# Optimization experiments

Measured on AMD Instinct MI355X. Metric: run time of the kernel, lower is better.

## Reference

```python
import jax, jax.numpy as jnp
import numpy as np

B, H, W = 512, 36, 36
N = H * W          # 1296 oscillators
K = 8              # couplings per oscillator
EP0 = 0.1          # kura_update_rate
ANNEAL = 0.5


def setup_inputs() -> dict:
    key = jax.random.key(0)
    k = jax.random.split(key, 8)
    return {
        "input": jax.random.normal(k[0], (B, H, W), jnp.float32),
        "initial_phase": jax.random.uniform(k[1], (B, N), jnp.float32) * (2.0 * np.pi),
        "connectivity": jax.random.randint(k[2], (B, N, K), 0, N),
        "episodes": 25,
        "conv1_w": jax.random.normal(k[3], (8, 1, 3, 3), jnp.float32) * 0.1,
        "conv1_b": jnp.zeros((8,), jnp.float32),
        "conv2_w": jax.random.normal(k[4], (16, 8, 3, 3), jnp.float32) * 0.1,
        "conv2_b": jnp.zeros((16,), jnp.float32),
        "conv3_w": jax.random.normal(k[5], (32, 16, 3, 3), jnp.float32) * 0.1,
        "conv3_b": jnp.zeros((32,), jnp.float32),
        "fc_w": jax.random.normal(k[6], (108 * 8, 108 * 32), jnp.float32) * 0.02,
        "fc_b": jnp.zeros((108 * 8,), jnp.float32),
    }


def _conv3x3(x, w, b):
    y = jax.lax.conv_general_dilated(
        x, w, (1, 1), "SAME", dimension_numbers=("NCHW", "OIHW", "NCHW"))
    return y + b[None, :, None, None]


def _kuramoto(initial_phase, coupling, connectivity, steps, ep0):
    # phase: [B,N]; coupling: [B,N,K]; connectivity: [B,N,K] neighbor indices
    gather = jax.vmap(lambda p, c: p[c])  # -> [B,N,K] neighbor phases

    def step(carry, i):
        phase, ep = carry
        neigh = gather(phase, connectivity)
        # d(phase_i) = ep * sum_j coupling_ij * sin(phase_j - phase_i)
        delta = ep * (coupling * jnp.sin(neigh - phase[:, :, None])).sum(-1)
        phase = phase + delta
        ep = ep - ANNEAL * i * ep / steps  # annealed update rate
        return (phase, ep), phase

    (_, _), phases = jax.lax.scan(
        step, (initial_phase, jnp.float32(ep0)),
        jnp.arange(steps, dtype=jnp.float32))
    # record=True: trajectory includes the initial phase
    return jnp.concatenate([initial_phase[None], phases], axis=0)  # [steps+1,B,N]


def reference(input, initial_phase, connectivity, episodes,
              conv1_w, conv1_b, conv2_w, conv2_b, conv3_w, conv3_b, fc_w, fc_b):
    x = input.reshape(-1, 1, 36, 36)
    c1 = jax.nn.relu(_conv3x3(x, conv1_w, conv1_b))
    c2 = jax.nn.relu(_conv3x3(c1, conv2_w, conv2_b))
    c3 = jax.nn.sigmoid(_conv3x3(c2, conv3_w, conv3_b))
    fc = (c3.reshape(-1, 108 * 32) @ fc_w.T + fc_b).reshape(-1, N, K)  # [B,1296,8]
    phase_list = _kuramoto(initial_phase, fc, connectivity, episodes, EP0)
    return phase_list, fc
```

## Files before the change

### kernel.cpp

```cpp
#include <hip/hip_runtime.h>
#include <hip/hip_bf16.h>

#define NPOS 1296
#define BATCH 512
#define STEPS 25
#define PH_STRIDE (BATCH * NPOS)
#define PH_TOTAL ((STEPS + 1) * PH_STRIDE)
#define FC_K 3456
#define FC_N 864
#define FC_NPAD 896
#define FC_M 6144

typedef float f32x4 __attribute__((ext_vector_type(4)));
typedef __bf16 bf16x8 __attribute__((ext_vector_type(8)));

__device__ __forceinline__ ushort f2bf(float f) {
  union { float f; unsigned u; } v; v.f = f;
  unsigned r = v.u + 0x7FFFu + ((v.u >> 16) & 1u);
  return (ushort)(r >> 16);
}
__device__ __forceinline__ float bf2f(ushort h) {
  union { unsigned u; float f; } v; v.u = ((unsigned)h) << 16; return v.f;
}

__device__ __forceinline__ void async_copy16(void* lds, const void* g) {
  __builtin_amdgcn_global_load_lds(
      (const __attribute__((address_space(1))) unsigned*)g,
      (__attribute__((address_space(3))) unsigned*)lds, 16, 0, 0);
}

__global__ __launch_bounds__(256) void wprep_kernel(
    const float* __restrict__ w1, const float* __restrict__ w2, const float* __restrict__ w3,
    float* __restrict__ w1t, ushort* __restrict__ w2t, ushort* __restrict__ w3t) {
  const int tid = threadIdx.x;
  for (int i = tid; i < 72; i += 256) {
    const int s = i / 8, co = i - s * 8;
    w1t[i] = w1[co * 9 + s];
  }
  for (int i = tid; i < 16 * 96; i += 256) {
    const int co = i / 96, k = i - co * 96;
    const int s = k / 8, ci = k - s * 8;
    w2t[i] = (k < 72) ? f2bf(w2[(co * 8 + ci) * 9 + s]) : (ushort)0;
  }
  for (int i = tid; i < 32 * 160; i += 256) {
    const int co = i / 160, k = i - co * 160;
    const int s = k / 16, ci = k - s * 16;
    w3t[i] = (k < 144) ? f2bf(w3[(co * 16 + ci) * 9 + s]) : (ushort)0;
  }
}

__global__ __launch_bounds__(256, 4) void conv_fused_kernel(
    const float* __restrict__ in, const float* __restrict__ w1t, const float* __restrict__ b1,
    const ushort* __restrict__ w2t, const float* __restrict__ b2,
    const ushort* __restrict__ w3t, const float* __restrict__ b3,
    ushort* __restrict__ aout) {
  __shared__ __align__(16) float sIn[18][40];
  __shared__ __align__(16) ushort sC1[18][40][8];
  __shared__ __align__(16) ushort sC2[16][40][16];
  const int b = blockIdx.x, band = blockIdx.y, tid = threadIdx.x;
  const int r0 = band * 12;
  const int wave = tid >> 6, lane = tid & 63;
  const int quad = lane >> 4, l16 = lane & 15;
  {
    const uint4 zz = make_uint4(0, 0, 0, 0);
    for (int i = tid; i < 180; i += 256) ((uint4*)sIn)[i] = zz;
    for (int i = tid; i < 720; i += 256) ((uint4*)sC1)[i] = zz;
    for (int i = tid; i < 1280; i += 256) ((uint4*)sC2)[i] = zz;
  }
  __syncthreads();
  for (int i = tid; i < 18 * 18; i += 256) {
    const int r = i / 18, c = i - r * 18;
    const int gy = r0 - 3 + r;
    if ((unsigned)gy < 36u)
      *(float2*)&sIn[r][2 + 2 * c] = *(const float2*)(in + (size_t)b * NPOS + gy * 36 + 2 * c);
  }
  __syncthreads();
  for (int i = tid; i < 16 * 36; i += 256) {
    const int lr = i / 36, x = i - lr * 36;
    float acc[8];
#pragma unroll
    for (int co = 0; co < 8; ++co) acc[co] = b1[co];
#pragma unroll
    for (int s = 0; s < 9; ++s) {
      const int dy = s / 3, dx = s - 3 * dy;
      const float v = sIn[lr + dy][x + 1 + dx];
#pragma unroll
      for (int co = 0; co < 8; ++co) acc[co] = fmaf(w1t[s * 8 + co], v, acc[co]);
    }
    const int g1 = r0 - 2 + lr;
    if ((unsigned)g1 < 36u) {
      uint4 pk;
      pk.x = (uint)f2bf(fmaxf(acc[0], 0.f)) | ((uint)f2bf(fmaxf(acc[1], 0.f)) << 16);
      pk.y = (uint)f2bf(fmaxf(acc[2], 0.f)) | ((uint)f2bf(fmaxf(acc[3], 0.f)) << 16);
      pk.z = (uint)f2bf(fmaxf(acc[4], 0.f)) | ((uint)f2bf(fmaxf(acc[5], 0.f)) << 16);
      pk.w = (uint)f2bf(fmaxf(acc[6], 0.f)) | ((uint)f2bf(fmaxf(acc[7], 0.f)) << 16);
      *(uint4*)&sC1[lr][x + 2][0] = pk;
    }
  }
  __syncthreads();
  bf16x8 w2f[3];
#pragma unroll
  for (int f = 0; f < 3; ++f)
    w2f[f] = *(const bf16x8*)(w2t + l16 * 96 + f * 32 + quad * 8);
  const float bias2 = b2[l16];
  for (int chunk = wave; chunk < 32; chunk += 4) {
    const int m = chunk * 16 + l16;
    const int oy = m / 36, x = m - oy * 36;
    f32x4 acc = {0.f, 0.f, 0.f, 0.f};
#pragma unroll
    for (int f = 0; f < 3; ++f) {
      const int s0 = 4 * f + quad;
      const int dy = s0 / 3, dx = s0 - 3 * dy;
      const bf16x8 af = *(const bf16x8*)&sC1[oy + dy][x + 1 + dx][0];
      acc = __builtin_amdgcn_mfma_f32_16x16x32_bf16(af, w2f[f], acc, 0, 0, 0);
    }
#pragma unroll
    for (int r = 0; r < 4; ++r) {
      const int px = chunk * 16 + quad * 4 + r;
      const int oy2 = px / 36, x2 = px - oy2 * 36;
      const int g2 = r0 - 1 + oy2;
      if (px < 504 && (unsigned)g2 < 36u)
        sC2[oy2][x2 + 2][l16] = f2bf(fmaxf(acc[r] + bias2, 0.f));
    }
  }
  __syncthreads();
  bf16x8 w3f[2][5];
#pragma unroll
  for (int t = 0; t < 2; ++t)
#pragma unroll
    for (int f = 0; f < 5; ++f)
      w3f[t][f] = *(const bf16x8*)(w3t + (t * 16 + l16) * 160 + f * 32 + quad * 8);
  const float bias3a = b3[l16], bias3b = b3[16 + l16];
  ushort* ob = aout + (size_t)b * (32 * NPOS) + r0 * 36;
  for (int chunk = wave; chunk < 27; chunk += 4) {
    const int m = chunk * 16 + l16;
    const int oy = m / 36, x = m - oy * 36;
    f32x4 acc0 = {0.f, 0.f, 0.f, 0.f}, acc1 = {0.f, 0.f, 0.f, 0.f};
#pragma unroll
    for (int f = 0; f < 5; ++f) {
      const int s0 = 2 * f + (quad >> 1);
      const int dy = s0 / 3, dx = s0 - 3 * dy;
      const bf16x8 af = *(const bf16x8*)&sC2[oy + dy][x + 1 + dx][(quad & 1) * 8];
      acc0 = __builtin_amdgcn_mfma_f32_16x16x32_bf16(af, w3f[0][f], acc0, 0, 0, 0);
      acc1 = __builtin_amdgcn_mfma_f32_16x16x32_bf16(af, w3f[1][f], acc1, 0, 0, 0);
    }
    const int pxb = chunk * 16 + quad * 4;
    ushort4 pk;
#pragma unroll
    for (int r = 0; r < 4; ++r)
      ((ushort*)&pk)[r] = f2bf(1.f / (1.f + __expf(-(acc0[r] + bias3a))));
    *(ushort4*)(ob + (size_t)l16 * NPOS + pxb) = pk;
#pragma unroll
    for (int r = 0; r < 4; ++r)
      ((ushort*)&pk)[r] = f2bf(1.f / (1.f + __expf(-(acc1[r] + bias3b))));
    *(ushort4*)(ob + (size_t)(16 + l16) * NPOS + pxb) = pk;
  }
}

__global__ __launch_bounds__(256) void wcvt_kernel(const float* __restrict__ w, ushort* __restrict__ wb) {
  const int idx = blockIdx.x * 256 + threadIdx.x;
  if (idx >= FC_NPAD * FC_K) return;
  const int n = idx / FC_K;
  wb[idx] = (n < FC_N) ? f2bf(w[idx]) : (ushort)0;
}

__global__ __launch_bounds__(256) void gemm_kernel(
    const ushort* __restrict__ A, const ushort* __restrict__ Bt,
    const float* __restrict__ bias, float* __restrict__ C) {
  __shared__ __align__(16) ushort sA[2][96 * 32];
  __shared__ __align__(16) ushort sB[2][128 * 32];
  const int tid = threadIdx.x;
  const int lin = blockIdx.x;
  const int xcd = lin & 7, g = lin >> 3;
  const int bn = g % 7;
  const int bm = xcd + 8 * (g / 7);
  const int row0 = bm * 96, col0 = bn * 128;
  const int wave = tid >> 6, lane = tid & 63;
  const int wr = (wave >> 1) * 48, wc = (wave & 1) * 64;
  const int quad = lane >> 4, l16 = lane & 15;
  f32x4 acc[3][4] = {};
  const ushort* Asrc  = A  + ((size_t)row0 + (tid >> 2)) * FC_K + (tid & 3) * 8;
  const ushort* Asrc2 = Asrc + (size_t)64 * FC_K;
  const ushort* Bsrc  = Bt + ((size_t)col0 + (tid >> 2)) * FC_K + (tid & 3) * 8;
  const ushort* Bsrc2 = Bsrc + (size_t)64 * FC_K;
  const int halfwave = (tid < 128);
  for (int kt = 0; kt < FC_K / 64; ++kt) {
    const int k0 = kt * 64;
    __syncthreads();
#pragma unroll
    for (int s = 0; s < 2; ++s) {
      const int off = k0 + s * 32;
      async_copy16(sA[s] + wave * 512, Asrc + off);
      async_copy16(sB[s] + wave * 512, Bsrc + off);
      async_copy16(sB[s] + 2048 + wave * 512, Bsrc2 + off);
      if (halfwave) async_copy16(sA[s] + 2048 + wave * 512, Asrc2 + off);
    }
    __syncthreads();
#pragma unroll
    for (int s = 0; s < 2; ++s) {
      bf16x8 af[3], bfr[4];
#pragma unroll
      for (int t = 0; t < 3; ++t)
        af[t] = *(const bf16x8*)(sA[s] + (wr + t * 16 + l16) * 32 + quad * 8);
#pragma unroll
      for (int t = 0; t < 4; ++t)
        bfr[t] = *(const bf16x8*)(sB[s] + (wc + t * 16 + l16) * 32 + quad * 8);
#pragma unroll
      for (int tm = 0; tm < 3; ++tm)
#pragma unroll
        for (int tn = 0; tn < 4; ++tn)
          acc[tm][tn] = __builtin_amdgcn_mfma_f32_16x16x32_bf16(af[tm], bfr[tn], acc[tm][tn], 0, 0, 0);
    }
  }
#pragma unroll
  for (int tn = 0; tn < 4; ++tn) {
    const int col = col0 + wc + tn * 16 + l16;
    if (col < FC_N) {
      const float bv = bias[col];
#pragma unroll
      for (int tm = 0; tm < 3; ++tm) {
#pragma unroll
        for (int r = 0; r < 4; ++r) {
          const int row = row0 + wr + tm * 16 + quad * 4 + r;
          C[(size_t)row * FC_N + col] = acc[tm][tn][r] + bv;
        }
      }
    }
  }
}

__global__ __launch_bounds__(512) void kuramoto_kernel(
    const float* __restrict__ ph0, const int* __restrict__ conn,
    const float* __restrict__ cpl, float* __restrict__ out) {
  __shared__ float ph[NPOS];
  __shared__ float2 sc[NPOS];
  const int b = blockIdx.x, tid = threadIdx.x;
  int rj[3][8];
  float rc[3][8];
#pragma unroll
  for (int s = 0; s < 3; ++s) {
    const int i = tid + s * 512;
    if (i < NPOS) {
      const float p = ph0[(size_t)b * NPOS + i];
      ph[i] = p;
      __builtin_nontemporal_store(p, out + (size_t)b * NPOS + i);
      const size_t base = (size_t)b * (NPOS * 8) + (size_t)i * 8;
      const int4 j0 = *(const int4*)(conn + base);
      const int4 j1 = *(const int4*)(conn + base + 4);
      const float4 c0 = *(const float4*)(cpl + base);
      const float4 c1 = *(const float4*)(cpl + base + 4);
      rj[s][0] = j0.x; rj[s][1] = j0.y; rj[s][2] = j0.z; rj[s][3] = j0.w;
      rj[s][4] = j1.x; rj[s][5] = j1.y; rj[s][6] = j1.z; rj[s][7] = j1.w;
      rc[s][0] = c0.x; rc[s][1] = c0.y; rc[s][2] = c0.z; rc[s][3] = c0.w;
      rc[s][4] = c1.x; rc[s][5] = c1.y; rc[s][6] = c1.z; rc[s][7] = c1.w;
    } else {
#pragma unroll
      for (int k = 0; k < 8; ++k) { rj[s][k] = 0; rc[s][k] = 0.f; }
    }
  }
  float ep = 0.1f;
  for (int t = 0; t < STEPS; ++t) {
    __syncthreads();
    for (int i = tid; i < NPOS; i += 512) {
      float s, c;
      __sincosf(ph[i], &s, &c);
      sc[i] = make_float2(s, c);
    }
    __syncthreads();
    float* op = out + (size_t)(t + 1) * PH_STRIDE + (size_t)b * NPOS;
#pragma unroll
    for (int s = 0; s < 3; ++s) {
      const int i = tid + s * 512;
      if (i < NPOS) {
        float ss = 0.f, cs = 0.f;
#pragma unroll
        for (int k = 0; k < 8; ++k) {
          const float2 v = sc[rj[s][k]];
          ss = fmaf(rc[s][k], v.x, ss);
          cs = fmaf(rc[s][k], v.y, cs);
        }
        const float2 me = sc[i];
        const float np = ph[i] + ep * (me.y * ss - me.x * cs);
        ph[i] = np;
        __builtin_nontemporal_store(np, op + i);
      }
    }
    ep = ep * (1.0f - 0.02f * (float)t);
  }
}

extern "C" void kernel_launch(void* const* d_in, const int* in_sizes, int n_in,
                              void* d_out, int out_size, void* d_ws, size_t ws_size,
                              hipStream_t stream) {
  const float* input = (const float*)d_in[0];
  const float* ph0   = (const float*)d_in[1];
  const int*   conn  = (const int*)d_in[2];
  const float* w1 = (const float*)d_in[4];
  const float* b1 = (const float*)d_in[5];
  const float* w2 = (const float*)d_in[6];
  const float* b2 = (const float*)d_in[7];
  const float* w3 = (const float*)d_in[8];
  const float* b3 = (const float*)d_in[9];
  const float* fcw = (const float*)d_in[10];
  const float* fcb = (const float*)d_in[11];
  float* out = (float*)d_out;

  ushort* Abuf = (ushort*)d_ws;
  ushort* Wbuf = (ushort*)((char*)d_ws + 42467328);
  float*  w1t  = (float*)((char*)d_ws + 48660480);
  ushort* w2t  = (ushort*)((char*)d_ws + 48660768);
  ushort* w3t  = (ushort*)((char*)d_ws + 48663840);
  float* fcout = out + PH_TOTAL;

  wprep_kernel<<<1, 256, 0, stream>>>(w1, w2, w3, w1t, w2t, w3t);
  wcvt_kernel<<<(FC_NPAD * FC_K) / 256, 256, 0, stream>>>(fcw, Wbuf);
  conv_fused_kernel<<<dim3(BATCH, 3), 256, 0, stream>>>(input, w1t, b1, w2t, b2, w3t, b3, Abuf);
  gemm_kernel<<<448, 256, 0, stream>>>(Abuf, Wbuf, fcb, fcout);
  kuramoto_kernel<<<BATCH, 512, 0, stream>>>(ph0, conn, fcout, out);
}
```

Baseline: 268.8 us.

## Pipeline GEMM loads with vmcnt waits and swizzled LDS; double-buffer Kuramoto sincos

The GEMM now keeps two K-tiles in flight. It issues global-to-LDS copies for tile k+2 right after computing tile k, and it waits with s_waitcnt vmcnt(7) plus a raw barrier instead of two full __syncthreads. It also XOR-swizzles the LDS layout to cut bank conflicts. The Kuramoto kernel keeps each oscillator's phase and sin/cos in registers and writes sin/cos into a ping-pong LDS buffer. This removes one barrier and the separate sincos pass per step. The wrap-around prefetch loads redundant tiles at the end, and the hand-written waitcnt logic depends on the compiler not reordering the memory operations.

```diff
diff --git a/kernel.cpp b/kernel.cpp
--- a/kernel.cpp
+++ b/kernel.cpp
@@ -10,6 +10,7 @@
 #define FC_N 864
 #define FC_NPAD 896
 #define FC_M 6144
+#define KT_ITERS 54
 
 typedef float f32x4 __attribute__((ext_vector_type(4)));
 typedef __bf16 bf16x8 __attribute__((ext_vector_type(8)));
@@ -28,6 +29,9 @@
       (const __attribute__((address_space(1))) unsigned*)g,
       (__attribute__((address_space(3))) unsigned*)lds, 16, 0, 0);
 }
+__device__ __forceinline__ void raw_barrier() { asm volatile("s_barrier" ::: "memory"); }
+__device__ __forceinline__ void waitcnt_vm7() { asm volatile("s_waitcnt vmcnt(7)" ::: "memory"); }
+__device__ __forceinline__ void waitcnt_vm0() { asm volatile("s_waitcnt vmcnt(0)" ::: "memory"); }
 
 __global__ __launch_bounds__(256) void wprep_kernel(
     const float* __restrict__ w1, const float* __restrict__ w2, const float* __restrict__ w3,
@@ -167,8 +171,7 @@
 __global__ __launch_bounds__(256) void gemm_kernel(
     const ushort* __restrict__ A, const ushort* __restrict__ Bt,
     const float* __restrict__ bias, float* __restrict__ C) {
-  __shared__ __align__(16) ushort sA[2][96 * 32];
-  __shared__ __align__(16) ushort sB[2][128 * 32];
+  __shared__ __align__(16) ushort smem[2][14336];
   const int tid = threadIdx.x;
   const int lin = blockIdx.x;
   const int xcd = lin & 7, g = lin >> 3;
@@ -178,40 +181,65 @@
   const int wave = tid >> 6, lane = tid & 63;
   const int wr = (wave >> 1) * 48, wc = (wave & 1) * 64;
   const int quad = lane >> 4, l16 = lane & 15;
+  const int oswz = (quad ^ ((l16 >> 1) & 3)) * 8;
   f32x4 acc[3][4] = {};
-  const ushort* Asrc  = A  + ((size_t)row0 + (tid >> 2)) * FC_K + (tid & 3) * 8;
-  const ushort* Asrc2 = Asrc + (size_t)64 * FC_K;
-  const ushort* Bsrc  = Bt + ((size_t)col0 + (tid >> 2)) * FC_K + (tid & 3) * 8;
-  const ushort* Bsrc2 = Bsrc + (size_t)64 * FC_K;
-  const int halfwave = (tid < 128);
-  for (int kt = 0; kt < FC_K / 64; ++kt) {
-    const int k0 = kt * 64;
-    __syncthreads();
-#pragma unroll
-    for (int s = 0; s < 2; ++s) {
-      const int off = k0 + s * 32;
-      async_copy16(sA[s] + wave * 512, Asrc + off);
-      async_copy16(sB[s] + wave * 512, Bsrc + off);
-      async_copy16(sB[s] + 2048 + wave * 512, Bsrc2 + off);
-      if (halfwave) async_copy16(sA[s] + 2048 + wave * 512, Asrc2 + off);
-    }
-    __syncthreads();
+
+  const int rr = lane >> 2;
+  const int soct = ((lane & 3) ^ ((lane >> 3) & 3)) * 8;
+  const ushort* gsrc[7];
+  const ushort* ldst[7];
+  {
+    const int s = wave >> 1;
+    if ((wave & 1) == 0) {
+#pragma unroll
+      for (int j = 0; j < 6; ++j) {
+        gsrc[j] = A + ((size_t)row0 + j * 16 + rr) * FC_K + s * 32 + soct;
+        ldst[j] = &smem[0][s * 3072 + j * 512];
+      }
+      gsrc[6] = Bt + ((size_t)col0 + rr) * FC_K + s * 32 + soct;
+      ldst[6] = &smem[0][6144 + s * 4096];
+    } else {
+#pragma unroll
+      for (int j = 0; j < 7; ++j) {
+        gsrc[j] = Bt + ((size_t)col0 + (j + 1) * 16 + rr) * FC_K + s * 32 + soct;
+        ldst[j] = &smem[0][6144 + s * 4096 + (j + 1) * 512];
+      }
+    }
+  }
+#pragma unroll
+  for (int j = 0; j < 7; ++j) async_copy16((void*)ldst[j], gsrc[j]);
+#pragma unroll
+  for (int j = 0; j < 7; ++j) async_copy16((void*)(ldst[j] + 14336), gsrc[j] + 64);
+
+  for (int kt = 0; kt < KT_ITERS; ++kt) {
+    const int p = kt & 1;
+    waitcnt_vm7();
+    raw_barrier();
+    const ushort* base = &smem[p][0];
 #pragma unroll
     for (int s = 0; s < 2; ++s) {
       bf16x8 af[3], bfr[4];
 #pragma unroll
       for (int t = 0; t < 3; ++t)
-        af[t] = *(const bf16x8*)(sA[s] + (wr + t * 16 + l16) * 32 + quad * 8);
+        af[t] = *(const bf16x8*)(base + s * 3072 + (wr + t * 16 + l16) * 32 + oswz);
 #pragma unroll
       for (int t = 0; t < 4; ++t)
-        bfr[t] = *(const bf16x8*)(sB[s] + (wc + t * 16 + l16) * 32 + quad * 8);
+        bfr[t] = *(const bf16x8*)(base + 6144 + s * 4096 + (wc + t * 16 + l16) * 32 + oswz);
 #pragma unroll
       for (int tm = 0; tm < 3; ++tm)
 #pragma unroll
         for (int tn = 0; tn < 4; ++tn)
           acc[tm][tn] = __builtin_amdgcn_mfma_f32_16x16x32_bf16(af[tm], bfr[tn], acc[tm][tn], 0, 0, 0);
     }
-  }
+    raw_barrier();
+    int kn = kt + 2;
+    if (kn >= KT_ITERS) kn -= KT_ITERS;
+    const int koff = kn * 64;
+#pragma unroll
+    for (int j = 0; j < 7; ++j) async_copy16((void*)(ldst[j] + p * 14336), gsrc[j] + koff);
+  }
+  waitcnt_vm0();
+
 #pragma unroll
   for (int tn = 0; tn < 4; ++tn) {
     const int col = col0 + wc + tn * 16 + l16;
@@ -232,18 +260,23 @@
 __global__ __launch_bounds__(512) void kuramoto_kernel(
     const float* __restrict__ ph0, const int* __restrict__ conn,
     const float* __restrict__ cpl, float* __restrict__ out) {
-  __shared__ float ph[NPOS];
-  __shared__ float2 sc[NPOS];
+  __shared__ float2 sc[2][NPOS];
   const int b = blockIdx.x, tid = threadIdx.x;
   int rj[3][8];
   float rc[3][8];
+  float myph[3];
+  float2 mysc[3];
 #pragma unroll
   for (int s = 0; s < 3; ++s) {
     const int i = tid + s * 512;
     if (i < NPOS) {
       const float p = ph0[(size_t)b * NPOS + i];
-      ph[i] = p;
+      myph[s] = p;
       __builtin_nontemporal_store(p, out + (size_t)b * NPOS + i);
+      float sn, cn;
+      __sincosf(p, &sn, &cn);
+      mysc[s] = make_float2(sn, cn);
+      sc[0][i] = mysc[s];
       const size_t base = (size_t)b * (NPOS * 8) + (size_t)i * 8;
       const int4 j0 = *(const int4*)(conn + base);
       const int4 j1 = *(const int4*)(conn + base + 4);
@@ -253,36 +286,31 @@
       rj[s][4] = j1.x; rj[s][5] = j1.y; rj[s][6] = j1.z; rj[s][7] = j1.w;
       rc[s][0] = c0.x; rc[s][1] = c0.y; rc[s][2] = c0.z; rc[s][3] = c0.w;
       rc[s][4] = c1.x; rc[s][5] = c1.y; rc[s][6] = c1.z; rc[s][7] = c1.w;
-    } else {
-#pragma unroll
-      for (int k = 0; k < 8; ++k) { rj[s][k] = 0; rc[s][k] = 0.f; }
     }
   }
   float ep = 0.1f;
   for (int t = 0; t < STEPS; ++t) {
     __syncthreads();
-    for (int i = tid; i < NPOS; i += 512) {
-      float s, c;
-      __sincosf(ph[i], &s, &c);
-      sc[i] = make_float2(s, c);
-    }
-    __syncthreads();
+    const int cur = t & 1;
     float* op = out + (size_t)(t + 1) * PH_STRIDE + (size_t)b * NPOS;
 #pragma unroll
     for (int s = 0; s < 3; ++s) {
       const int i = tid + s * 512;
       if (i < NPOS) {
-        float ss = 0.f, cs = 0.f;
+        float ss = 0.f, cc = 0.f;
 #pragma unroll
         for (int k = 0; k < 8; ++k) {
-          const float2 v = sc[rj[s][k]];
+          const float2 v = sc[cur][rj[s][k]];
           ss = fmaf(rc[s][k], v.x, ss);
-          cs = fmaf(rc[s][k], v.y, cs);
+          cc = fmaf(rc[s][k], v.y, cc);
         }
-        const float2 me = sc[i];
-        const float np = ph[i] + ep * (me.y * ss - me.x * cs);
-        ph[i] = np;
+        const float np = myph[s] + ep * (mysc[s].y * ss - mysc[s].x * cc);
+        myph[s] = np;
         __builtin_nontemporal_store(np, op + i);
+        float sn, cn;
+        __sincosf(np, &sn, &cn);
+        mysc[s] = make_float2(sn, cn);
+        sc[cur ^ 1][i] = mysc[s];
       }
     }
     ep = ep * (1.0f - 0.02f * (float)t);
```

Result: faster. 248.2 us (-7.7%).
